# Optimization experiments

Measured on AMD Instinct MI355X. Metric: run time of the kernel, lower is better.

## Reference

```python
import jax, jax.numpy as jnp
import numpy as np

# irreps_in = irreps_out = 32x0e + 16x1o ; irreps_sh = 1x0e + 1x1o
MUL0, MUL1 = 32, 16
N_NODES = 12000
N_EDGES = 120000
INV_SQRT3 = float(1.0 / np.sqrt(3.0))   # w3j(1,1,0), w3j(0,1,1), w3j(1,0,1) coefficient
SQRT2 = float(np.sqrt(2.0))             # e3nn normalize2mom constant for ReLU
# e3nn TP norms: irrep_normalization='component', path_normalization='element'.
# Each output irrep receives paths with num_elements 32 and 16 -> x = 48.
N_0E = float(1.0 / np.sqrt(48.0))       # alpha = dim(0e)/48 = 1/48
N_1O = float(np.sqrt(3.0 / 48.0))       # alpha = dim(1o)/48 = 3/48
# uvw weight blocks (mul2 = 1): (s,y0->s),(s,y0->g),(v,y1->s),(v,y1->g),(s,y1->v),(v,y0->v)
SPLITS = [MUL0 * MUL0, MUL0 * MUL1, MUL1 * MUL0, MUL1 * MUL1, MUL0 * MUL1, MUL1 * MUL1]
OFFS = np.cumsum([0] + SPLITS)
WNUM = int(OFFS[-1])  # 3072


def setup_inputs() -> dict:
    key = jax.random.key(0)
    k1, k2, k3, k4, k5 = jax.random.split(key, 5)
    x = jax.random.normal(k1, (N_NODES, MUL0 + 3 * MUL1), dtype=jnp.float32)
    edge_attr = jax.random.normal(k2, (N_EDGES, 64), dtype=jnp.float32)
    Yij = jax.random.normal(k3, (N_EDGES, 4), dtype=jnp.float32)
    edge_index = jax.random.randint(k4, (2, N_EDGES), 0, N_NODES, dtype=jnp.int64)
    w_emb = jax.random.normal(k5, (2 * MUL0 + 64, WNUM), dtype=jnp.float32)
    return {"x": x, "edge_attr": edge_attr, "Yij": Yij,
            "edge_index": edge_index, "w_emb": w_emb}


def reference(x, edge_attr, Yij, edge_index, w_emb):
    dst, src = edge_index[0], edge_index[1]
    E = edge_attr.shape[0]
    xs = x[:, :MUL0]                                   # [N, 32] scalars (0e)
    xv = x[:, MUL0:].reshape(-1, MUL1, 3)              # [N, 16, 3] vectors (1o)

    # per-edge weight MLP (single e3nn FC layer, weight scaled by 1/sqrt(fan_in))
    emb = jnp.concatenate([xs[dst], xs[src], edge_attr], axis=-1)     # [E, 128]
    w = emb @ (w_emb / np.sqrt(w_emb.shape[0]))                       # [E, 3072]
    Ws = [w[:, OFFS[i]:OFFS[i + 1]] for i in range(6)]
    W1 = Ws[0].reshape(E, MUL0, MUL0)
    W2 = Ws[1].reshape(E, MUL0, MUL1)
    W3 = Ws[2].reshape(E, MUL1, MUL0)
    W4 = Ws[3].reshape(E, MUL1, MUL1)
    W5 = Ws[4].reshape(E, MUL0, MUL1)
    W6 = Ws[5].reshape(E, MUL1, MUL1)

    # gather source features, split sh
    x1s, x1v = xs[src], xv[src]                        # [E,32], [E,16,3]
    y0, y1 = Yij[:, 0], Yij[:, 1:4]                    # [E], [E,3]

    sy0 = x1s * y0[:, None]                            # 0e x 0e paths
    vdot = jnp.einsum('euk,ek->eu', x1v, y1) * INV_SQRT3  # 1o x 1o -> 0e
    out_s = N_0E * (jnp.einsum('euw,eu->ew', W1, sy0) +
                    jnp.einsum('euw,eu->ew', W3, vdot))    # [E, 32]
    out_g = N_0E * (jnp.einsum('euw,eu->ew', W2, sy0) +
                    jnp.einsum('euw,eu->ew', W4, vdot))    # [E, 16]
    out_v = (N_1O * INV_SQRT3) * (
        jnp.einsum('euw,eu,ek->ewk', W5, x1s, y1) +
        jnp.einsum('euw,euk->ewk', W6, x1v * y0[:, None, None]))  # [E, 16, 3]

    msg = jnp.concatenate([out_s, out_g, out_v.reshape(E, MUL1 * 3)], axis=-1)  # [E, 96]

    # scatter mean onto destination nodes
    summed = jax.ops.segment_sum(msg, dst, num_segments=N_NODES)
    cnt = jax.ops.segment_sum(jnp.ones((E,), msg.dtype), dst, num_segments=N_NODES)
    mean = summed / jnp.maximum(cnt, 1.0)[:, None]

    # Gate (e3nn Activation normalizes ReLU by sqrt(2))
    s = SQRT2 * jax.nn.relu(mean[:, :MUL0])
    g = SQRT2 * jax.nn.relu(mean[:, MUL0:MUL0 + MUL1])
    v = mean[:, MUL0 + MUL1:].reshape(-1, MUL1, 3) * g[:, :, None]
    out = jnp.concatenate([s, v.reshape(-1, MUL1 * 3)], axis=-1)     # [N, 80]
    return x + out
```

## Files before the change

kernel.cpp:

```cpp
#include <hip/hip_runtime.h>
#include <hip/hip_bf16.h>

#define E_EDGES 120000
#define NUM_NODES 12000
#define N_WAVES 1875

typedef __attribute__((ext_vector_type(8))) short bfrag;
typedef __attribute__((ext_vector_type(8))) unsigned short ushort8;
typedef __attribute__((ext_vector_type(4))) float f32x4;

#define INV_SQRT3 0.57735026918962576f
#define SQRT2_C   1.41421356237309515f
#define N_0E_C    0.14433756729740643f
#define NV_C      0.14433756729740643f
#define WSCALE    0.08838834764831845f

__device__ __forceinline__ unsigned short f2bf(float f) {
    union { float f; unsigned int u; } v; v.f = f;
    unsigned int r = v.u + 0x7fffu + ((v.u >> 16) & 1u);
    return (unsigned short)(r >> 16);
}

__device__ __forceinline__ ushort8 pack8(f32x4 a, f32x4 b) {
    ushort8 o;
    o[0] = f2bf(a.x); o[1] = f2bf(a.y); o[2] = f2bf(a.z); o[3] = f2bf(a.w);
    o[4] = f2bf(b.x); o[5] = f2bf(b.y); o[6] = f2bf(b.z); o[7] = f2bf(b.w);
    return o;
}

__global__ void k_wt(const float* __restrict__ w_emb, unsigned short* __restrict__ Bt) {
    int i = blockIdx.x * 256 + threadIdx.x;
    if (i >= 128 * 3072) return;
    int k = i / 3072;
    int n = i - k * 3072;
    int t = n >> 4, col = n & 15;
    int kb = k >> 5, quad = (k >> 3) & 3, j = k & 7;
    Bt[(size_t)t * 2048 + (size_t)(kb * 64 + quad * 16 + col) * 8 + j] = f2bf(w_emb[i] * WSCALE);
}

__global__ void k_prep(const float* __restrict__ x, const float* __restrict__ edge_attr,
                       const float* __restrict__ Yij, const int* __restrict__ edge_index,
                       unsigned short* __restrict__ emb, float* __restrict__ rT,
                       float* __restrict__ cnt) {
    int e = blockIdx.x * 256 + threadIdx.x;
    if (e >= E_EDGES) return;
    int dst = edge_index[e];
    int src = edge_index[E_EDGES + e];
    f32x4 y = *(const f32x4*)(Yij + 4 * (long)e);
    float y0 = y.x, y1a = y.y, y1b = y.z, y1c = y.w;
    const float* xd = x + (long)dst * 80;
    const float* xs = x + (long)src * 80;
    const float* ea = edge_attr + (long)e * 64;

    ushort8* embp = (ushort8*)(emb + (long)e * 128);
    float* rb = rT + (size_t)(e >> 6) * 8192 + (e & 63);

    float xsv[80];
#pragma unroll
    for (int i = 0; i < 80; i += 4) {
        f32x4 v = *(const f32x4*)(xs + i);
        xsv[i] = v.x; xsv[i + 1] = v.y; xsv[i + 2] = v.z; xsv[i + 3] = v.w;
    }
#pragma unroll
    for (int cb = 0; cb < 4; ++cb) {
        f32x4 a = *(const f32x4*)(xd + cb * 8);
        f32x4 b = *(const f32x4*)(xd + cb * 8 + 4);
        embp[cb] = pack8(a, b);
    }
#pragma unroll
    for (int cb = 0; cb < 4; ++cb) {
        f32x4 a, b;
        a.x = xsv[cb * 8 + 0]; a.y = xsv[cb * 8 + 1]; a.z = xsv[cb * 8 + 2]; a.w = xsv[cb * 8 + 3];
        b.x = xsv[cb * 8 + 4]; b.y = xsv[cb * 8 + 5]; b.z = xsv[cb * 8 + 6]; b.w = xsv[cb * 8 + 7];
        embp[4 + cb] = pack8(a, b);
    }
#pragma unroll
    for (int cb = 0; cb < 8; ++cb) {
        f32x4 a = *(const f32x4*)(ea + cb * 8);
        f32x4 b = *(const f32x4*)(ea + cb * 8 + 4);
        embp[8 + cb] = pack8(a, b);
    }
#pragma unroll
    for (int u = 0; u < 32; ++u) rb[u * 64] = xsv[u] * y0;
#pragma unroll
    for (int u = 0; u < 16; ++u)
        rb[(32 + u) * 64] =
            (xsv[32 + 3 * u] * y1a + xsv[33 + 3 * u] * y1b + xsv[34 + 3 * u] * y1c) * INV_SQRT3;
#pragma unroll
    for (int u = 0; u < 32; ++u) rb[(48 + u) * 64] = xsv[u];
#pragma unroll
    for (int j = 0; j < 48; ++j) rb[(80 + j) * 64] = xsv[32 + j] * y0;
    atomicAdd(cnt + dst, 1.0f);
}

__global__ __launch_bounds__(256, 2) void k_gemm(
    const unsigned short* __restrict__ emb, const unsigned short* __restrict__ Bt,
    const float* __restrict__ rT, const int* __restrict__ edge_index,
    const float* __restrict__ Yij, float* __restrict__ summed) {
    const int lane = threadIdx.x & 63;
    const int wave = threadIdx.x >> 6;
    const int phase = blockIdx.x % 3;
    const int wid = (blockIdx.x / 3) * 4 + wave;
    if (wid >= N_WAVES) return;
    const long e0 = (long)wid * 64;
    const int col = lane & 15, quad = lane >> 4;

    bfrag A[4][4];
#pragma unroll
    for (int s = 0; s < 4; ++s) {
        const unsigned short* ap = emb + (e0 + s * 16 + col) * 128 + quad * 8;
#pragma unroll
        for (int kb = 0; kb < 4; ++kb) A[s][kb] = *(const bfrag*)(ap + kb * 32);
    }

    const float* rbase = rT + (size_t)wid * 8192 + quad * 4;
    auto loadw4 = [&](int r, f32x4* w) {
        const float* p = rbase + r * 64;
#pragma unroll
        for (int s = 0; s < 4; ++s) w[s] = *(const f32x4*)(p + s * 16);
    };
    auto loadB = [&](int t, bfrag* B) {
        const char* p = (const char*)Bt + (size_t)t * 4096 + lane * 16;
#pragma unroll
        for (int kb = 0; kb < 4; ++kb) B[kb] = *(const bfrag*)(p + kb * 1024);
    };

    f32x4 z = {0.f, 0.f, 0.f, 0.f};
    auto tileC = [&](const bfrag* B, f32x4* c) {
#pragma unroll
        for (int s = 0; s < 4; ++s) c[s] = z;
#pragma unroll
        for (int kb = 0; kb < 4; ++kb)
#pragma unroll
            for (int s = 0; s < 4; ++s)
                c[s] = __builtin_amdgcn_mfma_f32_16x16x32_bf16(A[s][kb], B[kb], c[s], 0, 0, 0);
    };

    if (phase == 0) {
        f32x4 acc0[4] = {z, z, z, z}, acc1[4] = {z, z, z, z};
        bfrag Ba[4], Bb[4], Na[4], Nb[4];
        f32x4 w[4], wn[4];
        loadB(0, Ba); loadB(1, Bb); loadw4(0, w);
#pragma unroll 1
        for (int p = 0; p < 48; ++p) {
            if (p < 47) {
                int tn = (p + 1 < 32) ? 2 * (p + 1) : 2 * (p + 1) + 32;
                loadB(tn, Na); loadB(tn + 1, Nb); loadw4(p + 1, wn);
            }
            f32x4 c[4];
            tileC(Ba, c);
#pragma unroll
            for (int s = 0; s < 4; ++s) acc0[s] += c[s] * w[s];
            tileC(Bb, c);
#pragma unroll
            for (int s = 0; s < 4; ++s) acc1[s] += c[s] * w[s];
#pragma unroll
            for (int i = 0; i < 4; ++i) { Ba[i] = Na[i]; Bb[i] = Nb[i]; w[i] = wn[i]; }
        }
#pragma unroll
        for (int s = 0; s < 4; ++s) {
            long eb = e0 + s * 16 + quad * 4;
#pragma unroll
            for (int r = 0; r < 4; ++r) {
                int d = edge_index[eb + r];
                float* base = summed + (long)d * 96;
                atomicAdd(base + col,      N_0E_C * acc0[s][r]);
                atomicAdd(base + col + 16, N_0E_C * acc1[s][r]);
            }
        }
    } else if (phase == 1) {
        f32x4 accg[4] = {z, z, z, z}, acct[4] = {z, z, z, z};
        bfrag B[4], Bn[4];
        f32x4 w[4], wn[4];
        loadB(64, B); loadw4(0, w);
#pragma unroll 1
        for (int i = 0; i < 80; ++i) {
            if (i < 79) {
                int j = i + 1;
                int tn = (j < 32) ? 64 + j : (j < 48 ? 96 + j : 96 + j);
                loadB(tn, Bn); loadw4(j, wn);
            }
            f32x4 c[4];
            tileC(B, c);
            if (i < 48) {
#pragma unroll
                for (int s = 0; s < 4; ++s) accg[s] += c[s] * w[s];
            } else {
#pragma unroll
                for (int s = 0; s < 4; ++s) acct[s] += c[s] * w[s];
            }
#pragma unroll
            for (int k = 0; k < 4; ++k) { B[k] = Bn[k]; w[k] = wn[k]; }
        }
#pragma unroll
        for (int s = 0; s < 4; ++s) {
            long eb = e0 + s * 16 + quad * 4;
#pragma unroll
            for (int r = 0; r < 4; ++r) {
                long e = eb + r;
                int d = edge_index[e];
                float* base = summed + (long)d * 96;
                float y1a = Yij[4 * e + 1], y1b = Yij[4 * e + 2], y1c = Yij[4 * e + 3];
                atomicAdd(base + 32 + col, N_0E_C * accg[s][r]);
                float t5 = NV_C * acct[s][r];
                atomicAdd(base + 48 + col * 3 + 0, t5 * y1a);
                atomicAdd(base + 48 + col * 3 + 1, t5 * y1b);
                atomicAdd(base + 48 + col * 3 + 2, t5 * y1c);
            }
        }
    } else {
        f32x4 accv[4][3] = {{z,z,z},{z,z,z},{z,z,z},{z,z,z}};
        bfrag B[4], Bn[4];
        loadB(176, B);
#pragma unroll 1
        for (int u = 0; u < 16; ++u) {
            if (u < 15) loadB(177 + u, Bn);
            f32x4 w0[4], w1[4], w2[4];
            loadw4(80 + 3 * u, w0); loadw4(81 + 3 * u, w1); loadw4(82 + 3 * u, w2);
            f32x4 c[4];
            tileC(B, c);
#pragma unroll
            for (int s = 0; s < 4; ++s) {
                accv[s][0] += c[s] * w0[s];
                accv[s][1] += c[s] * w1[s];
                accv[s][2] += c[s] * w2[s];
            }
#pragma unroll
            for (int k = 0; k < 4; ++k) B[k] = Bn[k];
        }
#pragma unroll
        for (int s = 0; s < 4; ++s) {
            long eb = e0 + s * 16 + quad * 4;
#pragma unroll
            for (int r = 0; r < 4; ++r) {
                int d = edge_index[eb + r];
                float* base = summed + (long)d * 96;
                atomicAdd(base + 48 + col * 3 + 0, NV_C * accv[s][0][r]);
                atomicAdd(base + 48 + col * 3 + 1, NV_C * accv[s][1][r]);
                atomicAdd(base + 48 + col * 3 + 2, NV_C * accv[s][2][r]);
            }
        }
    }
}

__global__ void k_final(const float* __restrict__ x, const float* __restrict__ summed,
                        const float* __restrict__ cnt, float* __restrict__ out) {
    int tid = blockIdx.x * 256 + threadIdx.x;
    if (tid >= NUM_NODES * 80) return;
    int n = tid / 80, c = tid % 80;
    float m = fmaxf(cnt[n], 1.0f);
    float inv = 1.0f / m;
    float val;
    if (c < 32) {
        val = SQRT2_C * fmaxf(summed[(long)n * 96 + c] * inv, 0.0f);
    } else {
        int j = c - 32;
        int w = j / 3;
        float g = SQRT2_C * fmaxf(summed[(long)n * 96 + 32 + w] * inv, 0.0f);
        val = summed[(long)n * 96 + 48 + j] * inv * g;
    }
    out[tid] = x[tid] + val;
}

extern "C" void kernel_launch(void* const* d_in, const int* in_sizes, int n_in,
                              void* d_out, int out_size, void* d_ws, size_t ws_size,
                              hipStream_t stream) {
    const float* x         = (const float*)d_in[0];
    const float* edge_attr = (const float*)d_in[1];
    const float* Yij       = (const float*)d_in[2];
    const int*   edge_index= (const int*)d_in[3];
    const float* w_emb     = (const float*)d_in[4];
    float* out = (float*)d_out;

    char* ws = (char*)d_ws;
    size_t off = 0;
    unsigned short* emb = (unsigned short*)(ws + off); off += (size_t)E_EDGES * 128 * 2;
    unsigned short* Bt  = (unsigned short*)(ws + off); off += (size_t)3072 * 128 * 2;
    off = (off + 255) & ~(size_t)255;
    float* rT     = (float*)(ws + off); off += (size_t)N_WAVES * 8192 * 4;
    size_t zoff = off;
    float* summed = (float*)(ws + off); off += (size_t)NUM_NODES * 96 * 4;
    float* cnt    = (float*)(ws + off); off += (size_t)NUM_NODES * 4;

    hipMemsetAsync(ws + zoff, 0, (size_t)NUM_NODES * 97 * 4, stream);
    k_wt  <<<(128 * 3072 + 255) / 256, 256, 0, stream>>>(w_emb, Bt);
    k_prep<<<(E_EDGES + 255) / 256, 256, 0, stream>>>(x, edge_attr, Yij, edge_index, emb, rT, cnt);
    int blocks_per_phase = (N_WAVES + 3) / 4;
    k_gemm<<<3 * blocks_per_phase, 256, 0, stream>>>(emb, Bt, rT, edge_index, Yij, summed);
    k_final<<<(NUM_NODES * 80 + 255) / 256, 256, 0, stream>>>(x, summed, cnt, out);
}
```

Measured before the change: 327.9 us.

## Stage shared weight tiles into LDS with async global_load_lds double buffering

Before this change, each wave loaded the B (weight) fragments it needed straight from global memory into registers. Now the four waves of a block cooperatively stage 16KB chunks of B into a double-buffered LDS region using global_load_lds, synchronized with __syncthreads, and every wave reads the shared chunk. This reduces redundant global and L2 traffic for B and frees registers. The last partial group is handled by clamping to a duplicated final 64-edge tile whose atomics are skipped. The tradeoffs are a block-wide barrier on every chunk and an extra LDS read for each fragment.

```diff
diff --git a/kernel.cpp b/kernel.cpp
--- a/kernel.cpp
+++ b/kernel.cpp
@@ -3,7 +3,7 @@
 
 #define E_EDGES 120000
 #define NUM_NODES 12000
-#define N_WAVES 1875
+#define N_GROUPS 469
 
 typedef __attribute__((ext_vector_type(8))) short bfrag;
 typedef __attribute__((ext_vector_type(8))) unsigned short ushort8;
@@ -100,10 +100,13 @@
     const int lane = threadIdx.x & 63;
     const int wave = threadIdx.x >> 6;
     const int phase = blockIdx.x % 3;
-    const int wid = (blockIdx.x / 3) * 4 + wave;
-    if (wid >= N_WAVES) return;
-    const long e0 = (long)wid * 64;
+    const int grp = blockIdx.x / 3;
+    long e0 = (long)grp * 256 + (long)wave * 64;
+    const bool dup = (e0 + 64 > E_EDGES);
+    if (dup) e0 = E_EDGES - 64;
     const int col = lane & 15, quad = lane >> 4;
+
+    __shared__ __align__(16) char lds[2][16384];
 
     bfrag A[4][4];
 #pragma unroll
@@ -113,50 +116,76 @@
         for (int kb = 0; kb < 4; ++kb) A[s][kb] = *(const bfrag*)(ap + kb * 32);
     }
 
-    const float* rbase = rT + (size_t)wid * 8192 + quad * 4;
+    int wp = 0, rp = 0;
+    auto stage = [&](int ci) {
+        const char* g = (const char*)Bt + (size_t)ci * 16384 + wave * 4096 + lane * 16;
+        char* l = &lds[(wp++) & 1][wave * 4096];
+#pragma unroll
+        for (int j = 0; j < 4; ++j)
+            __builtin_amdgcn_global_load_lds(
+                (const __attribute__((address_space(1))) unsigned int*)(g + j * 1024),
+                (__attribute__((address_space(3))) unsigned int*)(l + j * 1024), 16, 0, 0);
+    };
+    auto nextbuf = [&](int nxt) -> const char* {
+        __syncthreads();
+        if (nxt >= 0) stage(nxt);
+        return lds[(rp++) & 1];
+    };
+
+    f32x4 z = {0.f, 0.f, 0.f, 0.f};
+    const float* rbase = rT + (size_t)(e0 >> 6) * 8192 + quad * 4;
     auto loadw4 = [&](int r, f32x4* w) {
         const float* p = rbase + r * 64;
 #pragma unroll
         for (int s = 0; s < 4; ++s) w[s] = *(const f32x4*)(p + s * 16);
     };
-    auto loadB = [&](int t, bfrag* B) {
-        const char* p = (const char*)Bt + (size_t)t * 4096 + lane * 16;
-#pragma unroll
-        for (int kb = 0; kb < 4; ++kb) B[kb] = *(const bfrag*)(p + kb * 1024);
+
+    auto tileC = [&](const char* lt, f32x4* c) {
+        bfrag B0 = *(const bfrag*)(lt + lane * 16);
+        bfrag B1 = *(const bfrag*)(lt + lane * 16 + 1024);
+        bfrag B2 = *(const bfrag*)(lt + lane * 16 + 2048);
+        bfrag B3 = *(const bfrag*)(lt + lane * 16 + 3072);
+#pragma unroll
+        for (int s = 0; s < 4; ++s) c[s] = z;
+#pragma unroll
+        for (int s = 0; s < 4; ++s) c[s] = __builtin_amdgcn_mfma_f32_16x16x32_bf16(A[s][0], B0, c[s], 0, 0, 0);
+#pragma unroll
+        for (int s = 0; s < 4; ++s) c[s] = __builtin_amdgcn_mfma_f32_16x16x32_bf16(A[s][1], B1, c[s], 0, 0, 0);
+#pragma unroll
+        for (int s = 0; s < 4; ++s) c[s] = __builtin_amdgcn_mfma_f32_16x16x32_bf16(A[s][2], B2, c[s], 0, 0, 0);
+#pragma unroll
+        for (int s = 0; s < 4; ++s) c[s] = __builtin_amdgcn_mfma_f32_16x16x32_bf16(A[s][3], B3, c[s], 0, 0, 0);
     };
 
-    f32x4 z = {0.f, 0.f, 0.f, 0.f};
-    auto tileC = [&](const bfrag* B, f32x4* c) {
-#pragma unroll
-        for (int s = 0; s < 4; ++s) c[s] = z;
-#pragma unroll
-        for (int kb = 0; kb < 4; ++kb)
-#pragma unroll
-            for (int s = 0; s < 4; ++s)
-                c[s] = __builtin_amdgcn_mfma_f32_16x16x32_bf16(A[s][kb], B[kb], c[s], 0, 0, 0);
-    };
+    f32x4 c[4];
 
     if (phase == 0) {
         f32x4 acc0[4] = {z, z, z, z}, acc1[4] = {z, z, z, z};
-        bfrag Ba[4], Bb[4], Na[4], Nb[4];
-        f32x4 w[4], wn[4];
-        loadB(0, Ba); loadB(1, Bb); loadw4(0, w);
+        f32x4 wA[4], wB[4], nA[4], nB[4];
+        stage(0);
+        loadw4(0, wA); loadw4(1, wB);
 #pragma unroll 1
-        for (int p = 0; p < 48; ++p) {
-            if (p < 47) {
-                int tn = (p + 1 < 32) ? 2 * (p + 1) : 2 * (p + 1) + 32;
-                loadB(tn, Na); loadB(tn + 1, Nb); loadw4(p + 1, wn);
-            }
-            f32x4 c[4];
-            tileC(Ba, c);
-#pragma unroll
-            for (int s = 0; s < 4; ++s) acc0[s] += c[s] * w[s];
-            tileC(Bb, c);
-#pragma unroll
-            for (int s = 0; s < 4; ++s) acc1[s] += c[s] * w[s];
-#pragma unroll
-            for (int i = 0; i < 4; ++i) { Ba[i] = Na[i]; Bb[i] = Nb[i]; w[i] = wn[i]; }
-        }
+        for (int i = 0; i < 24; ++i) {
+            int nchunk = (i < 15) ? i + 1 : (i < 23 ? 24 + (i - 15) : -1);
+            const char* buf = nextbuf(nchunk);
+            int nr = (i < 15) ? 2 * i + 2 : (i < 23 ? 32 + 2 * (i - 15) : 0);
+            loadw4(nr, nA); loadw4(nr + 1, nB);
+            tileC(buf, c);
+#pragma unroll
+            for (int s = 0; s < 4; ++s) acc0[s] += c[s] * wA[s];
+            tileC(buf + 4096, c);
+#pragma unroll
+            for (int s = 0; s < 4; ++s) acc1[s] += c[s] * wA[s];
+            tileC(buf + 8192, c);
+#pragma unroll
+            for (int s = 0; s < 4; ++s) acc0[s] += c[s] * wB[s];
+            tileC(buf + 12288, c);
+#pragma unroll
+            for (int s = 0; s < 4; ++s) acc1[s] += c[s] * wB[s];
+#pragma unroll
+            for (int s = 0; s < 4; ++s) { wA[s] = nA[s]; wB[s] = nB[s]; }
+        }
+        if (dup) return;
 #pragma unroll
         for (int s = 0; s < 4; ++s) {
             long eb = e0 + s * 16 + quad * 4;
@@ -170,28 +199,47 @@
         }
     } else if (phase == 1) {
         f32x4 accg[4] = {z, z, z, z}, acct[4] = {z, z, z, z};
-        bfrag B[4], Bn[4];
-        f32x4 w[4], wn[4];
-        loadB(64, B); loadw4(0, w);
+        f32x4 wA[4], wB[4], nA[4], nB[4];
+        stage(16);
+        loadw4(0, wA); loadw4(1, wB);
 #pragma unroll 1
-        for (int i = 0; i < 80; ++i) {
-            if (i < 79) {
-                int j = i + 1;
-                int tn = (j < 32) ? 64 + j : (j < 48 ? 96 + j : 96 + j);
-                loadB(tn, Bn); loadw4(j, wn);
-            }
-            f32x4 c[4];
-            tileC(B, c);
-            if (i < 48) {
-#pragma unroll
-                for (int s = 0; s < 4; ++s) accg[s] += c[s] * w[s];
-            } else {
-#pragma unroll
-                for (int s = 0; s < 4; ++s) acct[s] += c[s] * w[s];
-            }
-#pragma unroll
-            for (int k = 0; k < 4; ++k) { B[k] = Bn[k]; w[k] = wn[k]; }
-        }
+        for (int i = 0; i < 20; ++i) {
+            int nchunk = (i < 7) ? 17 + i : (i < 11 ? 32 + (i - 7) : (i < 19 ? 36 + (i - 11) : -1));
+            const char* buf = nextbuf(nchunk);
+            int r0 = (i < 8) ? 4 * i : (i < 12 ? 32 + 4 * (i - 8) : 48 + 4 * (i - 12));
+#pragma unroll
+            for (int h = 0; h < 2; ++h) {
+                int nr;
+                if (h == 0) nr = r0 + 2;
+                else {
+                    int j = i + 1;
+                    nr = (j < 8) ? 4 * j : (j < 12 ? 32 + 4 * (j - 8) : (j < 20 ? 48 + 4 * (j - 12) : 0));
+                }
+                f32x4 cwA[4], cwB[4];
+#pragma unroll
+                for (int s = 0; s < 4; ++s) { cwA[s] = wA[s]; cwB[s] = wB[s]; }
+                loadw4(nr, nA); loadw4(nr + 1, nB);
+                tileC(buf + h * 8192, c);
+                if (i < 12) {
+#pragma unroll
+                    for (int s = 0; s < 4; ++s) accg[s] += c[s] * cwA[s];
+                } else {
+#pragma unroll
+                    for (int s = 0; s < 4; ++s) acct[s] += c[s] * cwA[s];
+                }
+                tileC(buf + h * 8192 + 4096, c);
+                if (i < 12) {
+#pragma unroll
+                    for (int s = 0; s < 4; ++s) accg[s] += c[s] * cwB[s];
+                } else {
+#pragma unroll
+                    for (int s = 0; s < 4; ++s) acct[s] += c[s] * cwB[s];
+                }
+#pragma unroll
+                for (int s = 0; s < 4; ++s) { wA[s] = nA[s]; wB[s] = nB[s]; }
+            }
+        }
+        if (dup) return;
 #pragma unroll
         for (int s = 0; s < 4; ++s) {
             long eb = e0 + s * 16 + quad * 4;
@@ -210,24 +258,25 @@
         }
     } else {
         f32x4 accv[4][3] = {{z,z,z},{z,z,z},{z,z,z},{z,z,z}};
-        bfrag B[4], Bn[4];
-        loadB(176, B);
+        stage(44);
 #pragma unroll 1
-        for (int u = 0; u < 16; ++u) {
-            if (u < 15) loadB(177 + u, Bn);
-            f32x4 w0[4], w1[4], w2[4];
-            loadw4(80 + 3 * u, w0); loadw4(81 + 3 * u, w1); loadw4(82 + 3 * u, w2);
-            f32x4 c[4];
-            tileC(B, c);
-#pragma unroll
-            for (int s = 0; s < 4; ++s) {
-                accv[s][0] += c[s] * w0[s];
-                accv[s][1] += c[s] * w1[s];
-                accv[s][2] += c[s] * w2[s];
-            }
-#pragma unroll
-            for (int k = 0; k < 4; ++k) B[k] = Bn[k];
-        }
+        for (int i = 0; i < 4; ++i) {
+            const char* buf = nextbuf(i < 3 ? 45 + i : -1);
+#pragma unroll
+            for (int t = 0; t < 4; ++t) {
+                int u = 4 * i + t;
+                f32x4 w0[4], w1[4], w2[4];
+                loadw4(80 + 3 * u, w0); loadw4(81 + 3 * u, w1); loadw4(82 + 3 * u, w2);
+                tileC(buf + t * 4096, c);
+#pragma unroll
+                for (int s = 0; s < 4; ++s) {
+                    accv[s][0] += c[s] * w0[s];
+                    accv[s][1] += c[s] * w1[s];
+                    accv[s][2] += c[s] * w2[s];
+                }
+            }
+        }
+        if (dup) return;
 #pragma unroll
         for (int s = 0; s < 4; ++s) {
             long eb = e0 + s * 16 + quad * 4;
@@ -277,7 +326,7 @@
     unsigned short* emb = (unsigned short*)(ws + off); off += (size_t)E_EDGES * 128 * 2;
     unsigned short* Bt  = (unsigned short*)(ws + off); off += (size_t)3072 * 128 * 2;
     off = (off + 255) & ~(size_t)255;
-    float* rT     = (float*)(ws + off); off += (size_t)N_WAVES * 8192 * 4;
+    float* rT     = (float*)(ws + off); off += (size_t)(E_EDGES / 64) * 8192 * 4;
     size_t zoff = off;
     float* summed = (float*)(ws + off); off += (size_t)NUM_NODES * 96 * 4;
     float* cnt    = (float*)(ws + off); off += (size_t)NUM_NODES * 4;
@@ -285,7 +334,6 @@
     hipMemsetAsync(ws + zoff, 0, (size_t)NUM_NODES * 97 * 4, stream);
     k_wt  <<<(128 * 3072 + 255) / 256, 256, 0, stream>>>(w_emb, Bt);
     k_prep<<<(E_EDGES + 255) / 256, 256, 0, stream>>>(x, edge_attr, Yij, edge_index, emb, rT, cnt);
-    int blocks_per_phase = (N_WAVES + 3) / 4;
-    k_gemm<<<3 * blocks_per_phase, 256, 0, stream>>>(emb, Bt, rT, edge_index, Yij, summed);
+    k_gemm<<<3 * N_GROUPS, 256, 0, stream>>>(emb, Bt, rT, edge_index, Yij, summed);
     k_final<<<(NUM_NODES * 80 + 255) / 256, 256, 0, stream>>>(x, summed, cnt, out);
 }
```

Result: faster. 321.4 us (-2.0%).
